# Kernel tuning notes

Hardware: AMD Instinct MI355X
Metric: run time of the kernel (lower is better)

The kernel has to match this reference:

```python
import jax, jax.numpy as jnp
import numpy as np

B, L = 2, 1024
DIM = 512
N_LAYERS = 2
D_STATE = 16
D_CONV = 4
D_INNER = 2 * DIM          # expand_factor=2
DT_RANK = (DIM + 15) // 16  # ceil(d_model/16) = 32
VOCAB = 32000


def _rmsnorm(x, w, eps=1e-5):
    return x * jax.lax.rsqrt(jnp.mean(x * x, axis=-1, keepdims=True) + eps) * w


def _causal_conv(x, w, b):
    # x: (B,L,D_INNER); depthwise causal conv along L, kernel D_CONV
    xt = jnp.transpose(x, (0, 2, 1))  # (B,C,L)
    y = jax.lax.conv_general_dilated(
        xt, w, window_strides=(1,), padding=[(D_CONV - 1, 0)],
        dimension_numbers=('NCH', 'OIH', 'NCH'), feature_group_count=D_INNER)
    return jnp.transpose(y, (0, 2, 1)) + b


def _ssm(x, xproj_w, dt_w, dt_b, A_log, Dp):
    # x: (B,L,D_INNER)
    A = -jnp.exp(A_log)  # (D_INNER, D_STATE)
    dbc = jnp.einsum('bld,rd->blr', x, xproj_w)  # (B,L,DT_RANK+2*D_STATE)
    delta = jax.nn.softplus(jnp.einsum('blr,dr->bld', dbc[..., :DT_RANK], dt_w) + dt_b)
    Bm = dbc[..., DT_RANK:DT_RANK + D_STATE]   # (B,L,D_STATE)
    Cm = dbc[..., DT_RANK + D_STATE:]          # (B,L,D_STATE)
    dA = jnp.exp(delta[..., None] * A)                       # (B,L,D_INNER,D_STATE)
    dBx = (delta * x)[..., None] * Bm[:, :, None, :]         # (B,L,D_INNER,D_STATE)

    def step(h, inp):
        a, b = inp
        h = a * h + b
        return h, h

    h0 = jnp.zeros((x.shape[0], D_INNER, D_STATE), x.dtype)
    _, hs = jax.lax.scan(step, h0, (jnp.swapaxes(dA, 0, 1), jnp.swapaxes(dBx, 0, 1)))
    y = jnp.einsum('lbds,bls->bld', hs, Cm) + Dp * x
    return y


def _block(h, rw, iw, cw, cb, xw, dw, db, Al, Dp, ow):
    r = _rmsnorm(h, rw)
    xz = jnp.einsum('bld,ed->ble', r, iw)  # (B,L,2*D_INNER)
    xin, z = jnp.split(xz, 2, axis=-1)
    xin = jax.nn.silu(_causal_conv(xin, cw, cb))
    y = _ssm(xin, xw, dw, db, Al, Dp) * jax.nn.silu(z)
    return h + jnp.einsum('ble,de->bld', y, ow)


def _forward(x, embed, rms_w, in_w, conv_w, conv_b, xproj_w, dt_w, dt_b, A_log, Dp, out_w, ln_g, ln_b, head_w, head_b):
    h = embed[x]  # (B,L,DIM)
    for l in range(N_LAYERS):
        h = _block(h, rms_w[l], in_w[l], conv_w[l], conv_b[l], xproj_w[l],
                   dt_w[l], dt_b[l], A_log[l], Dp[l], out_w[l])
    mu = jnp.mean(h, axis=-1, keepdims=True)
    var = jnp.mean((h - mu) ** 2, axis=-1, keepdims=True)
    hn = (h - mu) * jax.lax.rsqrt(var + 1e-5) * ln_g + ln_b
    return jnp.einsum('bld,vd->blv', hn, head_w) + head_b


def setup_inputs() -> dict:
    key = jax.random.key(0)
    ks = jax.random.split(key, 10)
    s = 0.02
    x = jax.random.randint(ks[0], (B, L), 0, VOCAB)
    embed = jax.random.normal(ks[1], (VOCAB, DIM), jnp.float32) * s
    rms_w = jnp.ones((N_LAYERS, DIM), jnp.float32)
    in_w = jax.random.normal(ks[2], (N_LAYERS, 2 * D_INNER, DIM), jnp.float32) * s
    conv_w = jax.random.normal(ks[3], (N_LAYERS, D_INNER, 1, D_CONV), jnp.float32) * s
    conv_b = jnp.zeros((N_LAYERS, D_INNER), jnp.float32)
    xproj_w = jax.random.normal(ks[4], (N_LAYERS, DT_RANK + 2 * D_STATE, D_INNER), jnp.float32) * s
    dt_w = jax.random.normal(ks[5], (N_LAYERS, D_INNER, DT_RANK), jnp.float32) * s
    dt_b = jax.random.normal(ks[6], (N_LAYERS, D_INNER), jnp.float32) * s
    A_log = jnp.log(jnp.broadcast_to(jnp.arange(1, D_STATE + 1, dtype=jnp.float32), (N_LAYERS, D_INNER, D_STATE)))
    Dp = jnp.ones((N_LAYERS, D_INNER), jnp.float32)
    out_w = jax.random.normal(ks[7], (N_LAYERS, DIM, D_INNER), jnp.float32) * s
    ln_g = jnp.ones((DIM,), jnp.float32)
    ln_b = jnp.zeros((DIM,), jnp.float32)
    head_w = jax.random.normal(ks[8], (VOCAB, DIM), jnp.float32) * s
    head_b = jnp.zeros((VOCAB,), jnp.float32)
    return dict(x=x, embed=embed, rms_w=rms_w, in_w=in_w, conv_w=conv_w, conv_b=conv_b,
                xproj_w=xproj_w, dt_w=dt_w, dt_b=dt_b, A_log=A_log, Dp=Dp, out_w=out_w,
                ln_g=ln_g, ln_b=ln_b, head_w=head_w, head_b=head_b)


def reference(x, embed, rms_w, in_w, conv_w, conv_b, xproj_w, dt_w, dt_b, A_log, Dp, out_w, ln_g, ln_b, head_w, head_b):
    return _forward(x, embed, rms_w, in_w, conv_w, conv_b, xproj_w, dt_w, dt_b,
                    A_log, Dp, out_w, ln_g, ln_b, head_w, head_b)
```

## Files before the change

kernel.cpp:

```cpp
#include <hip/hip_runtime.h>

typedef unsigned short u16;
typedef __attribute__((ext_vector_type(8))) __bf16 bf16x8;
typedef __attribute__((ext_vector_type(4))) float f32x4;

#define B_ 2
#define L_ 1024
#define DIM_ 512
#define DINNER_ 1024
#define DSTATE_ 16
#define DTRANK_ 32
#define VOCAB_ 32000
#define NCHUNK 64
#define CLEN 16

__device__ __forceinline__ u16 f2bf(float f) {
    union { float f; unsigned u; } x; x.f = f;
    unsigned r = x.u + 0x7FFFu + ((x.u >> 16) & 1u);
    return (u16)(r >> 16);
}

__global__ __launch_bounds__(256) void prep(const float* __restrict__ in_w,
                                            const float* __restrict__ out_w,
                                            const float* __restrict__ head_w,
                                            const float* __restrict__ dt_w,
                                            const int* __restrict__ x,
                                            const float* __restrict__ embed,
                                            const float* __restrict__ rw,
                                            u16* __restrict__ win,
                                            u16* __restrict__ wout,
                                            u16* __restrict__ whd,
                                            float* __restrict__ dtwT,
                                            float* __restrict__ h,
                                            u16* __restrict__ rbf) {
    int bk = blockIdx.x;
    int t = threadIdx.x;
    if (bk < 19072) {
        const int n1 = 524288;
        const int n2 = n1 + 262144;
        int i = bk * 256 + t;
        const float4* s; ushort4* d; int j;
        if (i < n1)      { s = (const float4*)in_w;   d = (ushort4*)win;  j = i; }
        else if (i < n2) { s = (const float4*)out_w;  d = (ushort4*)wout; j = i - n1; }
        else             { s = (const float4*)head_w; d = (ushort4*)whd;  j = i - n2; }
        float4 v = s[j];
        ushort4 o; o.x = f2bf(v.x); o.y = f2bf(v.y); o.z = f2bf(v.z); o.w = f2bf(v.w);
        d[j] = o;
    } else if (bk < 19328) {
        int bb = bk - 19072;
        int l = bb >> 7;
        int e = (bb & 127) * 256 + t;
        int r = e >> 10, d = e & 1023;
        dtwT[(size_t)l * 32768 + r * 1024 + d] = dt_w[(size_t)l * 32768 + d * 32 + r];
    } else {
        int wave = t >> 6, lane = t & 63;
        int row = (bk - 19328) * 4 + wave;
        int tok = x[row];
        const float4* s = (const float4*)(embed + (size_t)tok * DIM_);
        float4 v0 = s[lane], v1 = s[lane + 64];
        float4* hd = (float4*)(h + (size_t)row * DIM_);
        hd[lane] = v0;
        hd[lane + 64] = v1;
        float ss = v0.x*v0.x + v0.y*v0.y + v0.z*v0.z + v0.w*v0.w
                 + v1.x*v1.x + v1.y*v1.y + v1.z*v1.z + v1.w*v1.w;
        for (int m = 1; m < 64; m <<= 1) ss += __shfl_xor(ss, m);
        float rms = rsqrtf(ss * (1.0f / DIM_) + 1e-5f);
        const float4* w4 = (const float4*)rw;
        float4 w0 = w4[lane], w1 = w4[lane + 64];
        u16* o = rbf + (size_t)row * DIM_;
        ushort4 a, b;
        a.x = f2bf(v0.x * rms * w0.x); a.y = f2bf(v0.y * rms * w0.y);
        a.z = f2bf(v0.z * rms * w0.z); a.w = f2bf(v0.w * rms * w0.w);
        b.x = f2bf(v1.x * rms * w1.x); b.y = f2bf(v1.y * rms * w1.y);
        b.z = f2bf(v1.z * rms * w1.z); b.w = f2bf(v1.w * rms * w1.w);
        *(ushort4*)(o + lane * 4) = a;
        *(ushort4*)(o + 256 + lane * 4) = b;
    }
}

__global__ __launch_bounds__(256) void rmsnorm_bf16(const float* __restrict__ h,
                                                    const float* __restrict__ w,
                                                    u16* __restrict__ out) {
    int wave = threadIdx.x >> 6, lane = threadIdx.x & 63;
    int row = blockIdx.x * 4 + wave;
    const float4* r4 = (const float4*)(h + (size_t)row * DIM_);
    float4 v0 = r4[lane], v1 = r4[lane + 64];
    float ss = v0.x*v0.x + v0.y*v0.y + v0.z*v0.z + v0.w*v0.w
             + v1.x*v1.x + v1.y*v1.y + v1.z*v1.z + v1.w*v1.w;
    for (int m = 1; m < 64; m <<= 1) ss += __shfl_xor(ss, m);
    float rms = rsqrtf(ss * (1.0f / DIM_) + 1e-5f);
    const float4* w4 = (const float4*)w;
    float4 w0 = w4[lane], w1 = w4[lane + 64];
    u16* o = out + (size_t)row * DIM_;
    ushort4 a, b;
    a.x = f2bf(v0.x * rms * w0.x); a.y = f2bf(v0.y * rms * w0.y);
    a.z = f2bf(v0.z * rms * w0.z); a.w = f2bf(v0.w * rms * w0.w);
    b.x = f2bf(v1.x * rms * w1.x); b.y = f2bf(v1.y * rms * w1.y);
    b.z = f2bf(v1.z * rms * w1.z); b.w = f2bf(v1.w * rms * w1.w);
    *(ushort4*)(o + lane * 4) = a;
    *(ushort4*)(o + 256 + lane * 4) = b;
}

__global__ __launch_bounds__(256) void layernorm_bf16(const float* __restrict__ h,
                                                      const float* __restrict__ g,
                                                      const float* __restrict__ bta,
                                                      u16* __restrict__ out) {
    int wave = threadIdx.x >> 6, lane = threadIdx.x & 63;
    int row = blockIdx.x * 4 + wave;
    const float4* r4 = (const float4*)(h + (size_t)row * DIM_);
    float4 v0 = r4[lane], v1 = r4[lane + 64];
    float s = v0.x + v0.y + v0.z + v0.w + v1.x + v1.y + v1.z + v1.w;
    float ss = v0.x*v0.x + v0.y*v0.y + v0.z*v0.z + v0.w*v0.w
             + v1.x*v1.x + v1.y*v1.y + v1.z*v1.z + v1.w*v1.w;
    for (int m = 1; m < 64; m <<= 1) { s += __shfl_xor(s, m); ss += __shfl_xor(ss, m); }
    float mu = s * (1.0f / DIM_);
    float var = ss * (1.0f / DIM_) - mu * mu;
    float rs = rsqrtf(var + 1e-5f);
    const float4* g4 = (const float4*)g;
    const float4* b4 = (const float4*)bta;
    float4 g0 = g4[lane], g1 = g4[lane + 64];
    float4 b0 = b4[lane], b1 = b4[lane + 64];
    u16* o = out + (size_t)row * DIM_;
    ushort4 a, b;
    a.x = f2bf((v0.x - mu) * rs * g0.x + b0.x); a.y = f2bf((v0.y - mu) * rs * g0.y + b0.y);
    a.z = f2bf((v0.z - mu) * rs * g0.z + b0.z); a.w = f2bf((v0.w - mu) * rs * g0.w + b0.w);
    b.x = f2bf((v1.x - mu) * rs * g1.x + b1.x); b.y = f2bf((v1.y - mu) * rs * g1.y + b1.y);
    b.z = f2bf((v1.z - mu) * rs * g1.z + b1.z); b.w = f2bf((v1.w - mu) * rs * g1.w + b1.w);
    *(ushort4*)(o + lane * 4) = a;
    *(ushort4*)(o + 256 + lane * 4) = b;
}

template <int MODE>
__global__ __launch_bounds__(256) void gemm_bt(const u16* __restrict__ A,
                                               const u16* __restrict__ B,
                                               float* __restrict__ C,
                                               const float* __restrict__ bias,
                                               int M, int N, int K,
                                               int nbx, int swzq) {
    __shared__ u16 As[4][128 * 32];
    __shared__ u16 Bs[4][128 * 32];
    const int tid = threadIdx.x;
    const int wave = tid >> 6;
    const int lane = tid & 63;
    int lin = blockIdx.x;
    if (swzq) lin = (lin & 7) * swzq + (lin >> 3);
    const int m0 = (lin % nbx) * 128;
    const int n0 = (lin / nbx) * 128;
    const int wr = wave >> 1, wc = wave & 1;
    f32x4 acc[4][4] = {};

    const int sub = lane >> 2;
    const int slotL = lane & 3;
    const int fsub = (sub & 3) ^ ((sub >> 2) & 3);
    const int scol = (slotL ^ fsub) * 8;

    auto stage = [&](int buf, int kt) {
        int k0 = kt * 32;
        #pragma unroll
        for (int i = 0; i < 4; ++i) {
            int c = wave * 4 + i;
            const u16* src;
            u16* dst;
            if (c < 8) {
                int row = c * 16 + sub;
                src = A + (size_t)(m0 + row) * K + k0 + scol;
                dst = &As[buf][c * 512];
            } else {
                int cc = c - 8;
                int row = cc * 16 + sub;
                src = B + (size_t)(n0 + row) * K + k0 + scol;
                dst = &Bs[buf][cc * 512];
            }
            __builtin_amdgcn_global_load_lds((const __attribute__((address_space(1))) void*)src,
                                             (__attribute__((address_space(3))) void*)dst,
                                             16, 0, 0);
        }
    };

    const int nt = K / 32;
    stage(0, 0); stage(1, 1); stage(2, 2);

    const int fr = lane & 15;
    const int q = lane >> 4;
    const int fswz = (fr & 3) ^ ((fr >> 2) & 3);
    const int rdoff = ((q ^ fswz) * 8);

    for (int t = 0; t < nt; ++t) {
        if (t + 2 < nt)      asm volatile("s_waitcnt vmcnt(8)" ::: "memory");
        else if (t + 1 < nt) asm volatile("s_waitcnt vmcnt(4)" ::: "memory");
        else                 asm volatile("s_waitcnt vmcnt(0)" ::: "memory");
        __builtin_amdgcn_sched_barrier(0);
        __builtin_amdgcn_s_barrier();
        asm volatile("" ::: "memory");
        __builtin_amdgcn_sched_barrier(0);
        if (t + 3 < nt) stage((t + 3) & 3, t + 3);
        const u16* Ab = &As[t & 3][0];
        const u16* Bb = &Bs[t & 3][0];
        bf16x8 a[4], b[4];
        #pragma unroll
        for (int mi = 0; mi < 4; ++mi)
            a[mi] = *(const bf16x8*)(Ab + (wr * 64 + mi * 16 + fr) * 32 + rdoff);
        #pragma unroll
        for (int ni = 0; ni < 4; ++ni)
            b[ni] = *(const bf16x8*)(Bb + (wc * 64 + ni * 16 + fr) * 32 + rdoff);
        __builtin_amdgcn_s_setprio(1);
        #pragma unroll
        for (int mi = 0; mi < 4; ++mi)
            #pragma unroll
            for (int ni = 0; ni < 4; ++ni)
                acc[mi][ni] = __builtin_amdgcn_mfma_f32_16x16x32_bf16(a[mi], b[ni], acc[mi][ni], 0, 0, 0);
        __builtin_amdgcn_s_setprio(0);
    }

    const int cl = lane & 15;
    const int rq = (lane >> 4) * 4;
    #pragma unroll
    for (int mi = 0; mi < 4; ++mi) {
        #pragma unroll
        for (int ni = 0; ni < 4; ++ni) {
            int col = n0 + wc * 64 + ni * 16 + cl;
            #pragma unroll
            for (int rr = 0; rr < 4; ++rr) {
                int row = m0 + wr * 64 + mi * 16 + rq + rr;
                size_t idx = (size_t)row * N + col;
                float v = acc[mi][ni][rr];
                if (MODE == 2)      C[idx] = v + bias[col];
                else                C[idx] = v;
            }
        }
    }
}

__global__ __launch_bounds__(512) void gemm256(const u16* __restrict__ A,
                                               const u16* __restrict__ B,
                                               float* __restrict__ C,
                                               const float* __restrict__ bias,
                                               int M, int N, int K,
                                               int nbx, int swzq) {
    __shared__ u16 As[4][256 * 32];
    __shared__ u16 Bs[4][256 * 32];
    const int tid = threadIdx.x;
    const int wave = tid >> 6;
    const int lane = tid & 63;
    int lin = blockIdx.x;
    if (swzq) lin = (lin & 7) * swzq + (lin >> 3);
    const int m0 = (lin % nbx) * 256;
    const int n0 = (lin / nbx) * 256;
    const int wrM = wave >> 2;
    const int wcN = wave & 3;
    f32x4 acc[8][4] = {};

    const int sub = lane >> 2;
    const int slotL = lane & 3;
    const int fsub = (sub & 3) ^ ((sub >> 2) & 3);
    const int scol = (slotL ^ fsub) * 8;

    auto stage = [&](int buf, int kt) {
        int k0 = kt * 32;
        #pragma unroll
        for (int i = 0; i < 4; ++i) {
            int c = wave * 4 + i;
            const u16* src;
            u16* dst;
            if (c < 16) {
                int row = c * 16 + sub;
                src = A + (size_t)(m0 + row) * K + k0 + scol;
                dst = &As[buf][c * 512];
            } else {
                int cc = c - 16;
                int row = cc * 16 + sub;
                src = B + (size_t)(n0 + row) * K + k0 + scol;
                dst = &Bs[buf][cc * 512];
            }
            __builtin_amdgcn_global_load_lds((const __attribute__((address_space(1))) void*)src,
                                             (__attribute__((address_space(3))) void*)dst,
                                             16, 0, 0);
        }
    };

    const int nt = K / 32;
    stage(0, 0); stage(1, 1); stage(2, 2);

    const int fr = lane & 15;
    const int q = lane >> 4;
    const int fswz = (fr & 3) ^ ((fr >> 2) & 3);
    const int rdoff = ((q ^ fswz) * 8);

    for (int t = 0; t < nt; ++t) {
        if (t + 2 < nt)      asm volatile("s_waitcnt vmcnt(8)" ::: "memory");
        else if (t + 1 < nt) asm volatile("s_waitcnt vmcnt(4)" ::: "memory");
        else                 asm volatile("s_waitcnt vmcnt(0)" ::: "memory");
        __builtin_amdgcn_sched_barrier(0);
        __builtin_amdgcn_s_barrier();
        asm volatile("" ::: "memory");
        __builtin_amdgcn_sched_barrier(0);
        if (t + 3 < nt) stage((t + 3) & 3, t + 3);
        const u16* Ab = &As[t & 3][0];
        const u16* Bb = &Bs[t & 3][0];
        bf16x8 a[8], b[4];
        #pragma unroll
        for (int mi = 0; mi < 8; ++mi)
            a[mi] = *(const bf16x8*)(Ab + (wrM * 128 + mi * 16 + fr) * 32 + rdoff);
        #pragma unroll
        for (int ni = 0; ni < 4; ++ni)
            b[ni] = *(const bf16x8*)(Bb + (wcN * 64 + ni * 16 + fr) * 32 + rdoff);
        __builtin_amdgcn_s_setprio(1);
        #pragma unroll
        for (int mi = 0; mi < 8; ++mi)
            #pragma unroll
            for (int ni = 0; ni < 4; ++ni)
                acc[mi][ni] = __builtin_amdgcn_mfma_f32_16x16x32_bf16(a[mi], b[ni], acc[mi][ni], 0, 0, 0);
        __builtin_amdgcn_s_setprio(0);
    }

    const int cl = lane & 15;
    const int rq = (lane >> 4) * 4;
    #pragma unroll
    for (int mi = 0; mi < 8; ++mi) {
        #pragma unroll
        for (int ni = 0; ni < 4; ++ni) {
            int col = n0 + wcN * 64 + ni * 16 + cl;
            float bv = bias[col];
            #pragma unroll
            for (int rr = 0; rr < 4; ++rr) {
                int row = m0 + wrM * 128 + mi * 16 + rq + rr;
                C[(size_t)row * N + col] = acc[mi][ni][rr] + bv;
            }
        }
    }
}

template <int MODE>
__global__ __launch_bounds__(256) void gemm64(const u16* __restrict__ A,
                                              const u16* __restrict__ B,
                                              float* __restrict__ C,
                                              int M, int N, int K,
                                              int nbx, int swzq) {
    __shared__ u16 As[4][64 * 64];
    __shared__ u16 Bs[4][64 * 64];
    const int tid = threadIdx.x;
    const int wave = tid >> 6;
    const int lane = tid & 63;
    int lin = blockIdx.x;
    if (swzq) lin = (lin & 7) * swzq + (lin >> 3);
    const int m0 = (lin % nbx) * 64;
    const int n0 = (lin / nbx) * 64;
    const int wr = wave >> 1, wc = wave & 1;
    f32x4 acc[2][2] = {};

    const int crow = lane >> 3;
    const int scol = ((lane & 7) ^ crow) * 8;

    auto stage = [&](int buf, int kt) {
        int k0 = kt * 64;
        #pragma unroll
        for (int i = 0; i < 4; ++i) {
            int c = wave * 4 + i;
            const u16* src;
            u16* dst;
            if (c < 8) {
                int row = c * 8 + crow;
                src = A + (size_t)(m0 + row) * K + k0 + scol;
                dst = &As[buf][c * 512];
            } else {
                int cc = c - 8;
                int row = cc * 8 + crow;
                src = B + (size_t)(n0 + row) * K + k0 + scol;
                dst = &Bs[buf][cc * 512];
            }
            __builtin_amdgcn_global_load_lds((const __attribute__((address_space(1))) void*)src,
                                             (__attribute__((address_space(3))) void*)dst,
                                             16, 0, 0);
        }
    };

    const int nt = K / 64;
    stage(0, 0); stage(1, 1); stage(2, 2);

    const int fr = lane & 15;
    const int q = lane >> 4;

    for (int t = 0; t < nt; ++t) {
        if (t + 2 < nt)      asm volatile("s_waitcnt vmcnt(8)" ::: "memory");
        else if (t + 1 < nt) asm volatile("s_waitcnt vmcnt(4)" ::: "memory");
        else                 asm volatile("s_waitcnt vmcnt(0)" ::: "memory");
        __builtin_amdgcn_sched_barrier(0);
        __builtin_amdgcn_s_barrier();
        asm volatile("" ::: "memory");
        __builtin_amdgcn_sched_barrier(0);
        if (t + 3 < nt) stage((t + 3) & 3, t + 3);
        const u16* Ab = &As[t & 3][0];
        const u16* Bb = &Bs[t & 3][0];
        bf16x8 a[2][2], b[2][2];
        #pragma unroll
        for (int ki = 0; ki < 2; ++ki) {
            #pragma unroll
            for (int mi = 0; mi < 2; ++mi) {
                int row = wr * 32 + mi * 16 + fr;
                a[ki][mi] = *(const bf16x8*)(Ab + row * 64 + ((((ki << 2) + q) ^ (fr & 7)) * 8));
            }
            #pragma unroll
            for (int ni = 0; ni < 2; ++ni) {
                int row = wc * 32 + ni * 16 + fr;
                b[ki][ni] = *(const bf16x8*)(Bb + row * 64 + ((((ki << 2) + q) ^ (fr & 7)) * 8));
            }
        }
        __builtin_amdgcn_s_setprio(1);
        #pragma unroll
        for (int ki = 0; ki < 2; ++ki)
            #pragma unroll
            for (int mi = 0; mi < 2; ++mi)
                #pragma unroll
                for (int ni = 0; ni < 2; ++ni)
                    acc[mi][ni] = __builtin_amdgcn_mfma_f32_16x16x32_bf16(a[ki][mi], b[ki][ni], acc[mi][ni], 0, 0, 0);
        __builtin_amdgcn_s_setprio(0);
    }

    const int cl = lane & 15;
    const int rq = (lane >> 4) * 4;
    #pragma unroll
    for (int mi = 0; mi < 2; ++mi) {
        #pragma unroll
        for (int ni = 0; ni < 2; ++ni) {
            int col = n0 + wc * 32 + ni * 16 + cl;
            #pragma unroll
            for (int rr = 0; rr < 4; ++rr) {
                int row = m0 + wr * 32 + mi * 16 + rq + rr;
                size_t idx = (size_t)row * N + col;
                float v = acc[mi][ni][rr];
                if (MODE == 1)      C[idx] += v;
                else                C[idx] = v;
            }
        }
    }
}

__global__ __launch_bounds__(256) void conv_xproj_dt(const float* __restrict__ xz,
                                                     const float* __restrict__ cw,
                                                     const float* __restrict__ cb,
                                                     const float* __restrict__ xw,
                                                     const float* __restrict__ dtwT,
                                                     const float* __restrict__ dtb,
                                                     float* __restrict__ xc,
                                                     float* __restrict__ dbc,
                                                     float* __restrict__ delta) {
    __shared__ float sxc[8 * 1024];
    __shared__ float sxw[64 * 132];
    __shared__ float sred[4][8][68];
    __shared__ float sdbc[8][64];
    int t = threadIdx.x;
    int m0 = blockIdx.x * 8;
    #pragma unroll
    for (int i = 0; i < 32; ++i) {
        int idx = t + i * 256;
        int mi = idx >> 10, d = idx & 1023;
        int m = m0 + mi;
        int l = m & (L_ - 1);
        float acc = cb[d];
        #pragma unroll
        for (int j = 0; j < 4; ++j) {
            int ll = l - 3 + j;
            if (ll >= 0) acc = fmaf(cw[d * 4 + j], xz[(size_t)(m - 3 + j) * (2 * DINNER_) + d], acc);
        }
        float sv = acc / (1.0f + __expf(-acc));
        sxc[mi * 1024 + d] = sv;
        xc[(size_t)m * DINNER_ + d] = sv;
    }
    const int n = t & 63, kg = t >> 6;
    float acc8[8] = {};
    for (int kc = 0; kc < 8; ++kc) {
        __syncthreads();
        #pragma unroll
        for (int i = 0; i < 8; ++i) {
            int f = t + i * 256;
            int row = f >> 5, col4 = f & 31;
            *(float4*)(&sxw[row * 132 + col4 * 4]) =
                *(const float4*)(xw + (size_t)row * DINNER_ + kc * 128 + col4 * 4);
        }
        __syncthreads();
        #pragma unroll
        for (int k4i = 0; k4i < 8; ++k4i) {
            int k4 = kg * 8 + k4i;
            float4 wv = *(const float4*)(&sxw[n * 132 + k4 * 4]);
            #pragma unroll
            for (int mi = 0; mi < 8; ++mi) {
                float4 xv = *(const float4*)(&sxc[mi * 1024 + kc * 128 + k4 * 4]);
                acc8[mi] += wv.x * xv.x + wv.y * xv.y + wv.z * xv.z + wv.w * xv.w;
            }
        }
    }
    #pragma unroll
    for (int mi = 0; mi < 8; ++mi) sred[kg][mi][n] = acc8[mi];
    __syncthreads();
    #pragma unroll
    for (int rep = 0; rep < 2; ++rep) {
        int o = t + rep * 256;
        int mi = o >> 6, n2 = o & 63;
        float v = sred[0][mi][n2] + sred[1][mi][n2] + sred[2][mi][n2] + sred[3][mi][n2];
        sdbc[mi][n2] = v;
        dbc[(size_t)(m0 + mi) * 64 + n2] = v;
    }
    __syncthreads();
    {
        int d0 = t * 4;
        float4 bias = *(const float4*)(dtb + d0);
        float4 am[8];
        #pragma unroll
        for (int mi = 0; mi < 8; ++mi) am[mi] = bias;
        const float4* wT = (const float4*)dtwT;
        #pragma unroll
        for (int r = 0; r < 32; ++r) {
            float4 wv = wT[r * 256 + t];
            #pragma unroll
            for (int mi = 0; mi < 8; ++mi) {
                float s = sdbc[mi][r];
                am[mi].x = fmaf(s, wv.x, am[mi].x);
                am[mi].y = fmaf(s, wv.y, am[mi].y);
                am[mi].z = fmaf(s, wv.z, am[mi].z);
                am[mi].w = fmaf(s, wv.w, am[mi].w);
            }
        }
        #pragma unroll
        for (int mi = 0; mi < 8; ++mi) {
            float4 o;
            o.x = (am[mi].x > 20.f) ? am[mi].x : log1pf(__expf(am[mi].x));
            o.y = (am[mi].y > 20.f) ? am[mi].y : log1pf(__expf(am[mi].y));
            o.z = (am[mi].z > 20.f) ? am[mi].z : log1pf(__expf(am[mi].z));
            o.w = (am[mi].w > 20.f) ? am[mi].w : log1pf(__expf(am[mi].w));
            *(float4*)(delta + (size_t)(m0 + mi) * DINNER_ + d0) = o;
        }
    }
}

__global__ __launch_bounds__(256) void ssm_part1(const float* __restrict__ delta,
                                                 const float* __restrict__ xc,
                                                 const float* __restrict__ dbc,
                                                 const float* __restrict__ A_log,
                                                 float* __restrict__ hfin,
                                                 float* __restrict__ sumd) {
    int tid = threadIdx.x;
    int d = blockIdx.x * 256 + tid;
    int c = blockIdx.y;
    int b = blockIdx.z;
    __shared__ float sB[CLEN][DSTATE_];
    {
        int l = tid >> 4, s = tid & 15;
        sB[l][s] = dbc[((size_t)(b * L_ + c * CLEN + l)) * 64 + DTRANK_ + s];
    }
    float A[16], h[16];
    {
        const float4* Ar = (const float4*)(A_log + (size_t)d * DSTATE_);
        #pragma unroll
        for (int i = 0; i < 4; ++i) {
            float4 al = Ar[i];
            A[i * 4 + 0] = -__expf(al.x); A[i * 4 + 1] = -__expf(al.y);
            A[i * 4 + 2] = -__expf(al.z); A[i * 4 + 3] = -__expf(al.w);
        }
    }
    #pragma unroll
    for (int s = 0; s < 16; ++s) h[s] = 0.f;
    __syncthreads();
    float sd = 0.f;
    size_t base = ((size_t)b * L_ + c * CLEN) * DINNER_ + d;
    #pragma unroll
    for (int l = 0; l < CLEN; ++l) {
        float dv = delta[base + (size_t)l * DINNER_];
        float xv = xc[base + (size_t)l * DINNER_];
        sd += dv;
        float dx = dv * xv;
        #pragma unroll
        for (int s = 0; s < 16; ++s) {
            float e = __expf(dv * A[s]);
            h[s] = fmaf(e, h[s], dx * sB[l][s]);
        }
    }
    float* hf = hfin + (((size_t)b * NCHUNK + c) * DINNER_ + d) * 16;
    #pragma unroll
    for (int i = 0; i < 4; ++i) {
        float4 v; v.x = h[i*4]; v.y = h[i*4+1]; v.z = h[i*4+2]; v.w = h[i*4+3];
        *(float4*)(hf + i * 4) = v;
    }
    sumd[((size_t)b * NCHUNK + c) * DINNER_ + d] = sd;
}

__global__ __launch_bounds__(256) void ssm_carry(const float* __restrict__ hfin,
                                                 const float* __restrict__ sumd,
                                                 const float* __restrict__ A_log,
                                                 float* __restrict__ h0buf) {
    int t = blockIdx.x * 256 + threadIdx.x;
    int s = t & 15;
    int dg = t >> 4;
    int d = dg & (DINNER_ - 1);
    int b = dg >> 10;
    float As = -__expf(A_log[(size_t)d * DSTATE_ + s]);
    float hc = 0.f;
    #pragma unroll 4
    for (int c = 0; c < NCHUNK; ++c) {
        size_t k = (((size_t)b * NCHUNK + c) * DINNER_ + d) * 16 + s;
        h0buf[k] = hc;
        float sdv = sumd[((size_t)b * NCHUNK + c) * DINNER_ + d];
        float hf = hfin[k];
        hc = fmaf(__expf(As * sdv), hc, hf);
    }
}

__global__ __launch_bounds__(256) void ssm_part2(const float* __restrict__ delta,
                                                 const float* __restrict__ xc,
                                                 const float* __restrict__ dbc,
                                                 const float* __restrict__ xz,
                                                 const float* __restrict__ A_log,
                                                 const float* __restrict__ Dp,
                                                 const float* __restrict__ h0buf,
                                                 u16* __restrict__ ys) {
    int tid = threadIdx.x;
    int d = blockIdx.x * 256 + tid;
    int c = blockIdx.y;
    int b = blockIdx.z;
    __shared__ float sBC[CLEN][32];
    {
        int l = tid >> 5, j = tid & 31;
        sBC[l][j] = dbc[((size_t)(b * L_ + c * CLEN + l)) * 64 + DTRANK_ + j];
        int e1 = tid + 256;
        l = e1 >> 5; j = e1 & 31;
        sBC[l][j] = dbc[((size_t)(b * L_ + c * CLEN + l)) * 64 + DTRANK_ + j];
    }
    float A[16], h[16];
    {
        const float4* Ar = (const float4*)(A_log + (size_t)d * DSTATE_);
        #pragma unroll
        for (int i = 0; i < 4; ++i) {
            float4 al = Ar[i];
            A[i * 4 + 0] = -__expf(al.x); A[i * 4 + 1] = -__expf(al.y);
            A[i * 4 + 2] = -__expf(al.z); A[i * 4 + 3] = -__expf(al.w);
        }
        const float4* h0 = (const float4*)(h0buf + (((size_t)b * NCHUNK + c) * DINNER_ + d) * 16);
        #pragma unroll
        for (int i = 0; i < 4; ++i) {
            float4 v = h0[i];
            h[i * 4 + 0] = v.x; h[i * 4 + 1] = v.y; h[i * 4 + 2] = v.z; h[i * 4 + 3] = v.w;
        }
    }
    float Dval = Dp[d];
    __syncthreads();
    size_t base = ((size_t)b * L_ + c * CLEN) * DINNER_ + d;
    size_t zbase = ((size_t)b * L_ + c * CLEN) * (2 * DINNER_) + DINNER_ + d;
    #pragma unroll
    for (int l = 0; l < CLEN; ++l) {
        float dv = delta[base + (size_t)l * DINNER_];
        float xv = xc[base + (size_t)l * DINNER_];
        float zv = xz[zbase + (size_t)l * (2 * DINNER_)];
        float dx = dv * xv;
        float y = 0.f;
        #pragma unroll
        for (int s = 0; s < 16; ++s) {
            float e = __expf(dv * A[s]);
            h[s] = fmaf(e, h[s], dx * sBC[l][s]);
            y = fmaf(h[s], sBC[l][16 + s], y);
        }
        y = fmaf(Dval, xv, y);
        float sg = zv / (1.0f + __expf(-zv));
        ys[base + (size_t)l * DINNER_] = f2bf(y * sg);
    }
}

extern "C" void kernel_launch(void* const* d_in, const int* in_sizes, int n_in,
                              void* d_out, int out_size, void* d_ws, size_t ws_size,
                              hipStream_t stream) {
    const int*   x       = (const int*)d_in[0];
    const float* embed   = (const float*)d_in[1];
    const float* rms_w   = (const float*)d_in[2];
    const float* in_w    = (const float*)d_in[3];
    const float* conv_w  = (const float*)d_in[4];
    const float* conv_b  = (const float*)d_in[5];
    const float* xproj_w = (const float*)d_in[6];
    const float* dt_w    = (const float*)d_in[7];
    const float* dt_b    = (const float*)d_in[8];
    const float* A_log   = (const float*)d_in[9];
    const float* Dp      = (const float*)d_in[10];
    const float* out_w   = (const float*)d_in[11];
    const float* ln_g    = (const float*)d_in[12];
    const float* ln_b    = (const float*)d_in[13];
    const float* head_w  = (const float*)d_in[14];
    const float* head_b  = (const float*)d_in[15];
    float* out = (float*)d_out;

    char* p = (char*)d_ws;
    auto take = [&](size_t n) { char* q = p; p += (n + 255) & ~(size_t)255; return q; };
    float* h    = (float*)take(2048ull * 512 * 4);
    u16*   r_bf = (u16*)  take(2048ull * 512 * 2);
    float* xz   = (float*)take(2048ull * 2048 * 4);
    float* xc   = (float*)take(2048ull * 1024 * 4);
    float* dbc  = (float*)take(2048ull * 64 * 4);
    float* dlt  = (float*)take(2048ull * 1024 * 4);
    u16*   ys   = (u16*)  take(2048ull * 1024 * 2);
    u16*   hn   = (u16*)  take(2048ull * 512 * 2);
    u16*   win  = (u16*)  take(2ull * 2048 * 512 * 2);
    u16*   wout = (u16*)  take(2ull * 512 * 1024 * 2);
    u16*   whd  = (u16*)  take(32000ull * 512 * 2);
    float* dtwT = (float*)take(2ull * 32 * 1024 * 4);
    float* hfin = (float*)take((size_t)B_ * NCHUNK * DINNER_ * 16 * 4);
    float* h0b  = (float*)take((size_t)B_ * NCHUNK * DINNER_ * 16 * 4);
    float* sumd = (float*)take((size_t)B_ * NCHUNK * DINNER_ * 4);

    prep<<<19840, 256, 0, stream>>>(in_w, out_w, head_w, dt_w, x, embed, rms_w,
                                    win, wout, whd, dtwT, h, r_bf);

    for (int l = 0; l < 2; ++l) {
        if (l > 0) rmsnorm_bf16<<<512, 256, 0, stream>>>(h, rms_w + l * DIM_, r_bf);
        gemm_bt<0><<<256, 256, 0, stream>>>(r_bf, win + (size_t)l * 2048 * 512, xz, nullptr, 2048, 2048, 512, 16, 32);
        conv_xproj_dt<<<256, 256, 0, stream>>>(xz, conv_w + l * DINNER_ * 4, conv_b + l * DINNER_,
                                               xproj_w + (size_t)l * 64 * 1024,
                                               dtwT + (size_t)l * 32 * 1024, dt_b + l * DINNER_,
                                               xc, dbc, dlt);
        ssm_part1<<<dim3(4, NCHUNK, B_), 256, 0, stream>>>(dlt, xc, dbc, A_log + (size_t)l * DINNER_ * DSTATE_, hfin, sumd);
        ssm_carry<<<128, 256, 0, stream>>>(hfin, sumd, A_log + (size_t)l * DINNER_ * DSTATE_, h0b);
        ssm_part2<<<dim3(4, NCHUNK, B_), 256, 0, stream>>>(dlt, xc, dbc, xz, A_log + (size_t)l * DINNER_ * DSTATE_,
                                                           Dp + l * DINNER_, h0b, ys);
        gemm64<1><<<256, 256, 0, stream>>>(ys, wout + (size_t)l * 512 * 1024, h, 2048, 512, 1024, 32, 32);
    }

    layernorm_bf16<<<512, 256, 0, stream>>>(h, ln_g, ln_b, hn);
    gemm256<<<1000, 512, 0, stream>>>(hn, whd, out, head_b, 2048, VOCAB_, 512, 8, 125);
}
```

Measured before the change: 361.7 us.

## Fuse chunked SSM scan passes and carry into one kernel with shared-memory state

Replaces the three SSM kernels (chunk-local scan, cross-chunk carry, second scan with output) with one kernel per (batch, 8-channel group). Each block scans all 64 chunks, keeps chunk-final states and delta sums in shared memory, propagates the carry there, then rescans to produce outputs. This drops two launches and the global round-trips of hfin/h0/sumd. In exchange, per-thread access to delta/xc becomes narrow (8 consecutive channels per 32-byte segment), which lowers coalescing. B/C now come from global loads instead of shared memory.

```diff
diff --git a/kernel.cpp b/kernel.cpp
--- a/kernel.cpp
+++ b/kernel.cpp
@@ -532,99 +532,23 @@
     }
 }
 
-__global__ __launch_bounds__(256) void ssm_part1(const float* __restrict__ delta,
-                                                 const float* __restrict__ xc,
-                                                 const float* __restrict__ dbc,
-                                                 const float* __restrict__ A_log,
-                                                 float* __restrict__ hfin,
-                                                 float* __restrict__ sumd) {
-    int tid = threadIdx.x;
-    int d = blockIdx.x * 256 + tid;
-    int c = blockIdx.y;
-    int b = blockIdx.z;
-    __shared__ float sB[CLEN][DSTATE_];
-    {
-        int l = tid >> 4, s = tid & 15;
-        sB[l][s] = dbc[((size_t)(b * L_ + c * CLEN + l)) * 64 + DTRANK_ + s];
-    }
-    float A[16], h[16];
-    {
-        const float4* Ar = (const float4*)(A_log + (size_t)d * DSTATE_);
-        #pragma unroll
-        for (int i = 0; i < 4; ++i) {
-            float4 al = Ar[i];
-            A[i * 4 + 0] = -__expf(al.x); A[i * 4 + 1] = -__expf(al.y);
-            A[i * 4 + 2] = -__expf(al.z); A[i * 4 + 3] = -__expf(al.w);
-        }
-    }
-    #pragma unroll
-    for (int s = 0; s < 16; ++s) h[s] = 0.f;
-    __syncthreads();
-    float sd = 0.f;
-    size_t base = ((size_t)b * L_ + c * CLEN) * DINNER_ + d;
-    #pragma unroll
-    for (int l = 0; l < CLEN; ++l) {
-        float dv = delta[base + (size_t)l * DINNER_];
-        float xv = xc[base + (size_t)l * DINNER_];
-        sd += dv;
-        float dx = dv * xv;
-        #pragma unroll
-        for (int s = 0; s < 16; ++s) {
-            float e = __expf(dv * A[s]);
-            h[s] = fmaf(e, h[s], dx * sB[l][s]);
-        }
-    }
-    float* hf = hfin + (((size_t)b * NCHUNK + c) * DINNER_ + d) * 16;
-    #pragma unroll
-    for (int i = 0; i < 4; ++i) {
-        float4 v; v.x = h[i*4]; v.y = h[i*4+1]; v.z = h[i*4+2]; v.w = h[i*4+3];
-        *(float4*)(hf + i * 4) = v;
-    }
-    sumd[((size_t)b * NCHUNK + c) * DINNER_ + d] = sd;
-}
-
-__global__ __launch_bounds__(256) void ssm_carry(const float* __restrict__ hfin,
-                                                 const float* __restrict__ sumd,
-                                                 const float* __restrict__ A_log,
-                                                 float* __restrict__ h0buf) {
-    int t = blockIdx.x * 256 + threadIdx.x;
-    int s = t & 15;
-    int dg = t >> 4;
-    int d = dg & (DINNER_ - 1);
-    int b = dg >> 10;
-    float As = -__expf(A_log[(size_t)d * DSTATE_ + s]);
-    float hc = 0.f;
-    #pragma unroll 4
-    for (int c = 0; c < NCHUNK; ++c) {
-        size_t k = (((size_t)b * NCHUNK + c) * DINNER_ + d) * 16 + s;
-        h0buf[k] = hc;
-        float sdv = sumd[((size_t)b * NCHUNK + c) * DINNER_ + d];
-        float hf = hfin[k];
-        hc = fmaf(__expf(As * sdv), hc, hf);
-    }
-}
-
-__global__ __launch_bounds__(256) void ssm_part2(const float* __restrict__ delta,
+__global__ __launch_bounds__(256) void ssm_fused(const float* __restrict__ delta,
                                                  const float* __restrict__ xc,
                                                  const float* __restrict__ dbc,
                                                  const float* __restrict__ xz,
                                                  const float* __restrict__ A_log,
                                                  const float* __restrict__ Dp,
-                                                 const float* __restrict__ h0buf,
                                                  u16* __restrict__ ys) {
-    int tid = threadIdx.x;
-    int d = blockIdx.x * 256 + tid;
-    int c = blockIdx.y;
-    int b = blockIdx.z;
-    __shared__ float sBC[CLEN][32];
-    {
-        int l = tid >> 5, j = tid & 31;
-        sBC[l][j] = dbc[((size_t)(b * L_ + c * CLEN + l)) * 64 + DTRANK_ + j];
-        int e1 = tid + 256;
-        l = e1 >> 5; j = e1 & 31;
-        sBC[l][j] = dbc[((size_t)(b * L_ + c * CLEN + l)) * 64 + DTRANK_ + j];
-    }
-    float A[16], h[16];
+    __shared__ float hfin[NCHUNK][8][16];
+    __shared__ float ssum[NCHUNK][8];
+    const int t = threadIdx.x;
+    const int b = blockIdx.x >> 7;
+    const int d0 = (blockIdx.x & 127) * 8;
+
+    const int dl = t & 7;
+    const int cp = t >> 3;
+    const int d = d0 + dl;
+    float A[16];
     {
         const float4* Ar = (const float4*)(A_log + (size_t)d * DSTATE_);
         #pragma unroll
@@ -633,33 +557,95 @@
             A[i * 4 + 0] = -__expf(al.x); A[i * 4 + 1] = -__expf(al.y);
             A[i * 4 + 2] = -__expf(al.z); A[i * 4 + 3] = -__expf(al.w);
         }
-        const float4* h0 = (const float4*)(h0buf + (((size_t)b * NCHUNK + c) * DINNER_ + d) * 16);
+    }
+    #pragma unroll
+    for (int u = 0; u < 2; ++u) {
+        int c = cp + u * 32;
+        size_t mrow = (size_t)b * L_ + c * CLEN;
+        size_t base = mrow * DINNER_ + d;
+        float h[16];
+        #pragma unroll
+        for (int s = 0; s < 16; ++s) h[s] = 0.f;
+        float sd = 0.f;
+        #pragma unroll
+        for (int l = 0; l < CLEN; ++l) {
+            float dv = delta[base + (size_t)l * DINNER_];
+            float xv = xc[base + (size_t)l * DINNER_];
+            const float4* B4 = (const float4*)(dbc + (mrow + l) * 64 + DTRANK_);
+            sd += dv;
+            float dx = dv * xv;
+            #pragma unroll
+            for (int i = 0; i < 4; ++i) {
+                float4 bv = B4[i];
+                h[i*4+0] = fmaf(__expf(dv * A[i*4+0]), h[i*4+0], dx * bv.x);
+                h[i*4+1] = fmaf(__expf(dv * A[i*4+1]), h[i*4+1], dx * bv.y);
+                h[i*4+2] = fmaf(__expf(dv * A[i*4+2]), h[i*4+2], dx * bv.z);
+                h[i*4+3] = fmaf(__expf(dv * A[i*4+3]), h[i*4+3], dx * bv.w);
+            }
+        }
         #pragma unroll
         for (int i = 0; i < 4; ++i) {
-            float4 v = h0[i];
-            h[i * 4 + 0] = v.x; h[i * 4 + 1] = v.y; h[i * 4 + 2] = v.z; h[i * 4 + 3] = v.w;
-        }
-    }
+            float4 v; v.x = h[i*4]; v.y = h[i*4+1]; v.z = h[i*4+2]; v.w = h[i*4+3];
+            *(float4*)(&hfin[c][dl][i * 4]) = v;
+        }
+        ssum[c][dl] = sd;
+    }
+    __syncthreads();
+
+    if (t < 128) {
+        int s = t & 15;
+        int dl2 = t >> 4;
+        float As_ = -__expf(A_log[(size_t)(d0 + dl2) * DSTATE_ + s]);
+        float hc = 0.f;
+        #pragma unroll 4
+        for (int c = 0; c < NCHUNK; ++c) {
+            float hf = hfin[c][dl2][s];
+            float sd = ssum[c][dl2];
+            hfin[c][dl2][s] = hc;
+            hc = fmaf(__expf(As_ * sd), hc, hf);
+        }
+    }
+    __syncthreads();
+
     float Dval = Dp[d];
-    __syncthreads();
-    size_t base = ((size_t)b * L_ + c * CLEN) * DINNER_ + d;
-    size_t zbase = ((size_t)b * L_ + c * CLEN) * (2 * DINNER_) + DINNER_ + d;
     #pragma unroll
-    for (int l = 0; l < CLEN; ++l) {
-        float dv = delta[base + (size_t)l * DINNER_];
-        float xv = xc[base + (size_t)l * DINNER_];
-        float zv = xz[zbase + (size_t)l * (2 * DINNER_)];
-        float dx = dv * xv;
-        float y = 0.f;
-        #pragma unroll
-        for (int s = 0; s < 16; ++s) {
-            float e = __expf(dv * A[s]);
-            h[s] = fmaf(e, h[s], dx * sBC[l][s]);
-            y = fmaf(h[s], sBC[l][16 + s], y);
-        }
-        y = fmaf(Dval, xv, y);
-        float sg = zv / (1.0f + __expf(-zv));
-        ys[base + (size_t)l * DINNER_] = f2bf(y * sg);
+    for (int u = 0; u < 2; ++u) {
+        int c = cp + u * 32;
+        size_t mrow = (size_t)b * L_ + c * CLEN;
+        size_t base = mrow * DINNER_ + d;
+        size_t zbase = mrow * (2 * DINNER_) + DINNER_ + d;
+        float h[16];
+        #pragma unroll
+        for (int i = 0; i < 4; ++i) {
+            float4 v = *(const float4*)(&hfin[c][dl][i * 4]);
+            h[i*4+0] = v.x; h[i*4+1] = v.y; h[i*4+2] = v.z; h[i*4+3] = v.w;
+        }
+        #pragma unroll
+        for (int l = 0; l < CLEN; ++l) {
+            float dv = delta[base + (size_t)l * DINNER_];
+            float xv = xc[base + (size_t)l * DINNER_];
+            float zv = xz[zbase + (size_t)l * (2 * DINNER_)];
+            const float4* B4 = (const float4*)(dbc + (mrow + l) * 64 + DTRANK_);
+            const float4* C4 = (const float4*)(dbc + (mrow + l) * 64 + DTRANK_ + DSTATE_);
+            float dx = dv * xv;
+            float y = 0.f;
+            #pragma unroll
+            for (int i = 0; i < 4; ++i) {
+                float4 bv = B4[i];
+                float4 cv = C4[i];
+                h[i*4+0] = fmaf(__expf(dv * A[i*4+0]), h[i*4+0], dx * bv.x);
+                h[i*4+1] = fmaf(__expf(dv * A[i*4+1]), h[i*4+1], dx * bv.y);
+                h[i*4+2] = fmaf(__expf(dv * A[i*4+2]), h[i*4+2], dx * bv.z);
+                h[i*4+3] = fmaf(__expf(dv * A[i*4+3]), h[i*4+3], dx * bv.w);
+                y = fmaf(h[i*4+0], cv.x, y);
+                y = fmaf(h[i*4+1], cv.y, y);
+                y = fmaf(h[i*4+2], cv.z, y);
+                y = fmaf(h[i*4+3], cv.w, y);
+            }
+            y = fmaf(Dval, xv, y);
+            float sg = zv / (1.0f + __expf(-zv));
+            ys[base + (size_t)l * DINNER_] = f2bf(y * sg);
+        }
     }
 }
 
@@ -698,9 +684,6 @@
     u16*   wout = (u16*)  take(2ull * 512 * 1024 * 2);
     u16*   whd  = (u16*)  take(32000ull * 512 * 2);
     float* dtwT = (float*)take(2ull * 32 * 1024 * 4);
-    float* hfin = (float*)take((size_t)B_ * NCHUNK * DINNER_ * 16 * 4);
-    float* h0b  = (float*)take((size_t)B_ * NCHUNK * DINNER_ * 16 * 4);
-    float* sumd = (float*)take((size_t)B_ * NCHUNK * DINNER_ * 4);
 
     prep<<<19840, 256, 0, stream>>>(in_w, out_w, head_w, dt_w, x, embed, rms_w,
                                     win, wout, whd, dtwT, h, r_bf);
@@ -712,10 +695,8 @@
                                                xproj_w + (size_t)l * 64 * 1024,
                                                dtwT + (size_t)l * 32 * 1024, dt_b + l * DINNER_,
                                                xc, dbc, dlt);
-        ssm_part1<<<dim3(4, NCHUNK, B_), 256, 0, stream>>>(dlt, xc, dbc, A_log + (size_t)l * DINNER_ * DSTATE_, hfin, sumd);
-        ssm_carry<<<128, 256, 0, stream>>>(hfin, sumd, A_log + (size_t)l * DINNER_ * DSTATE_, h0b);
-        ssm_part2<<<dim3(4, NCHUNK, B_), 256, 0, stream>>>(dlt, xc, dbc, xz, A_log + (size_t)l * DINNER_ * DSTATE_,
-                                                           Dp + l * DINNER_, h0b, ys);
+        ssm_fused<<<256, 256, 0, stream>>>(dlt, xc, dbc, xz, A_log + (size_t)l * DINNER_ * DSTATE_,
+                                           Dp + l * DINNER_, ys);
         gemm64<1><<<256, 256, 0, stream>>>(ys, wout + (size_t)l * 512 * 1024, h, 2048, 512, 1024, 32, 32);
     }
 
```

Result: slower. 402.6 us (+11.3%).
